# Optimization experiments

Hardware: AMD Instinct MI355X
Metric: run time of the kernel (lower is better)

Reference implementation:

```python
import jax, jax.numpy as jnp
import numpy as np

TOP_K = 2

def setup_inputs() -> dict:
    key = jax.random.key(0)
    k1, k2, k3, k4 = jax.random.split(key, 4)
    T, H, I, E = 8192, 2048, 4096, 8
    s = 0.02
    return {
        "hidden_states": jax.random.normal(k1, (T, H), dtype=jnp.float32),
        "router_w": jax.random.normal(k2, (E, H), dtype=jnp.float32) * s,
        "ws": jax.random.normal(k3, (E, 2 * I, H), dtype=jnp.float32) * s,  # [gate; up]
        "w2s": jax.random.normal(k4, (E, H, I), dtype=jnp.float32) * s,
    }

def reference(hidden_states, router_w, ws, w2s):
    # Router gating: softmax over experts, top-k, NO renormalization
    logits = hidden_states @ router_w.T              # [T, E]
    probs = jax.nn.softmax(logits, axis=-1)
    topv, topi = jax.lax.top_k(probs, TOP_K)         # [T, K]
    T, E = probs.shape
    I = w2s.shape[2]
    # Dense routing-weight matrix [T, E]; top_k indices are unique per token
    w = jnp.zeros_like(probs).at[jnp.arange(T)[:, None], topi].set(topv)
    out = jnp.zeros_like(hidden_states)
    for e in range(E):  # fixed small expert loop; avoids [T,E,2I] blowup
        gate = hidden_states @ ws[e, :I].T           # [T, I]
        up = hidden_states @ ws[e, I:].T             # [T, I]
        h = jax.nn.silu(gate) * up                   # SwiGLU
        out = out + w[:, e:e + 1] * (h @ w2s[e].T)   # combine
    return out
```

## Files before the change

### kernel.cpp

```cpp
#include <hip/hip_runtime.h>
#include <cstdint>
#include <cstddef>

#define T_TOK 8192
#define HDIM  2048
#define IDIM  4096
#define NEXP  8
#define MAXT  72

typedef __bf16 bf16x8 __attribute__((ext_vector_type(8)));
typedef float  f32x4  __attribute__((ext_vector_type(4)));

#define BARRIER() __builtin_amdgcn_s_barrier()
#define LGKM0()   do { asm volatile("s_waitcnt lgkmcnt(0)" ::: "memory"); __builtin_amdgcn_sched_barrier(0); } while (0)
#define VMW(n)    do { asm volatile("s_waitcnt vmcnt(" #n ")" ::: "memory"); } while (0)

__device__ __forceinline__ unsigned short f2bf(float f) {
    union { float f; unsigned u; } v; v.f = f;
    unsigned r = v.u + 0x7FFFu + ((v.u >> 16) & 1u);
    return (unsigned short)(r >> 16);
}

__device__ __forceinline__ void gload16(const void* g, void* l) {
    __builtin_amdgcn_global_load_lds((__attribute__((address_space(1))) void*)g,
                                     (__attribute__((address_space(3))) void*)l,
                                     16, 0, 0);
}

__global__ __launch_bounds__(256) void router_k(const float* __restrict__ hs,
                                                const float* __restrict__ rw,
                                                float* __restrict__ wgt,
                                                int* __restrict__ counts,
                                                int* __restrict__ lists) {
    int gid  = blockIdx.x * 256 + threadIdx.x;
    int tok  = gid >> 6;
    int lane = threadIdx.x & 63;
    const float* x = hs + (size_t)tok * HDIM;

    float acc[NEXP];
#pragma unroll
    for (int e = 0; e < NEXP; ++e) acc[e] = 0.f;
    for (int h = lane; h < HDIM; h += 64) {
        float xv = x[h];
#pragma unroll
        for (int e = 0; e < NEXP; ++e) acc[e] = fmaf(xv, rw[e * HDIM + h], acc[e]);
    }
#pragma unroll
    for (int off = 32; off > 0; off >>= 1) {
#pragma unroll
        for (int e = 0; e < NEXP; ++e) acc[e] += __shfl_xor(acc[e], off, 64);
    }
    if (lane == 0) {
        float m = acc[0];
#pragma unroll
        for (int e = 1; e < NEXP; ++e) m = fmaxf(m, acc[e]);
        float p[NEXP]; float s = 0.f;
#pragma unroll
        for (int e = 0; e < NEXP; ++e) { p[e] = expf(acc[e] - m); s += p[e]; }
        float inv = 1.f / s;
        int i1 = 0;
#pragma unroll
        for (int e = 1; e < NEXP; ++e) if (acc[e] > acc[i1]) i1 = e;
        int i2 = -1;
#pragma unroll
        for (int e = 0; e < NEXP; ++e) if (e != i1 && (i2 < 0 || acc[e] > acc[i2])) i2 = e;
#pragma unroll
        for (int e = 0; e < NEXP; ++e)
            wgt[(size_t)tok * NEXP + e] = (e == i1 || e == i2) ? p[e] * inv : 0.f;
        int p1 = atomicAdd(&counts[i1], 1);
        lists[i1 * T_TOK + p1] = tok;
        int p2 = atomicAdd(&counts[i2], 1);
        lists[i2 * T_TOK + p2] = (1 << 16) | tok;
    }
}

__global__ void plan_k(const int* __restrict__ counts, int* __restrict__ offs,
                       int* __restrict__ desc, int* __restrict__ ntiles) {
    if (threadIdx.x == 0 && blockIdx.x == 0) {
        int off = 0, n = 0;
        for (int e = 0; e < NEXP; ++e) {
            offs[e] = off;
            int nt = (counts[e] + 255) >> 8;
            for (int t = 0; t < nt; ++t) desc[n++] = (e << 16) | t;
            off += nt * 256;
        }
        *ntiles = n;
    }
}

__global__ __launch_bounds__(256) void cvt_k(const float* __restrict__ in,
                                             unsigned short* __restrict__ out, long n4) {
    long i      = (long)blockIdx.x * 256 + threadIdx.x;
    long stride = (long)gridDim.x * 256;
    const float4* in4 = (const float4*)in;
    ushort4* out4 = (ushort4*)out;
    for (long j = i; j < n4; j += stride) {
        float4 v = in4[j];
        ushort4 o;
        o.x = f2bf(v.x); o.y = f2bf(v.y); o.z = f2bf(v.z); o.w = f2bf(v.w);
        out4[j] = o;
    }
}

__global__ __launch_bounds__(512, 2) void gemm1_k(const unsigned short* __restrict__ A,
                                                  const unsigned short* __restrict__ Wall,
                                                  unsigned short* __restrict__ Hout,
                                                  const int* __restrict__ lists,
                                                  const int* __restrict__ counts,
                                                  const int* __restrict__ offs,
                                                  const int* __restrict__ desc,
                                                  const int* __restrict__ ntiles) {
    const int slot = blockIdx.y;
    if (slot >= *ntiles) return;
    const int dsc = desc[slot];
    const int e = dsc >> 16, tt = dsc & 0xFFFF;
    const int cnt = counts[e];
    const int t0 = tt * 256;
    const int* list = lists + e * T_TOK;
    const unsigned short* W = Wall + (size_t)e * 2 * IDIM * HDIM;
    const int hbase = offs[e];
    const int n0 = blockIdx.x * 128;

    extern __shared__ __align__(16) char lds[];

    const int tid  = threadIdx.x;
    const int lane = tid & 63;
    const int wid  = tid >> 6;
    const int wr   = wid >> 2;
    const int wc   = wid & 3;

    const int prow = tid >> 3;
    const int pcol = (tid & 7) * 16;
    const int fsw  = ((prow & 4) << 3) | ((prow & 8) << 3);
    const int lcol = (pcol ^ fsw) >> 1;
    unsigned aoff[4];
#pragma unroll
    for (int i = 0; i < 4; ++i) {
        int g = t0 + i * 64 + prow;
        int tok = list[(g < cnt) ? g : t0] & 0xFFFF;
        aoff[i] = (unsigned)tok * HDIM + lcol;
    }
    unsigned goff[2], uoff[2];
#pragma unroll
    for (int i = 0; i < 2; ++i) {
        goff[i] = (unsigned)(n0 + i * 64 + prow) * HDIM + lcol;
        uoff[i] = (unsigned)(IDIM + n0 + i * 64 + prow) * HDIM + lcol;
    }
    const int dst = tid * 16;

#define G1_STAGE(buf, kt) do {                                                     \
    unsigned k0_ = (unsigned)(kt) * 64;                                            \
    _Pragma("unroll") for (int i_ = 0; i_ < 4; ++i_)                               \
        gload16(A + aoff[i_] + k0_, lds + (buf) * 32768 + i_ * 8192 + dst);        \
    _Pragma("unroll") for (int i_ = 0; i_ < 2; ++i_)                               \
        gload16(W + goff[i_] + k0_, lds + 65536 + (buf) * 16384 + i_ * 8192 + dst);\
    _Pragma("unroll") for (int i_ = 0; i_ < 2; ++i_)                               \
        gload16(W + uoff[i_] + k0_, lds + 98304 + (buf) * 16384 + i_ * 8192 + dst);\
} while (0)

    const int frd = (lane & 12) << 3;
    const int cb0 = (((lane >> 4) * 16)      ) ^ frd;
    const int cb1 = (((lane >> 4) * 16) + 64 ) ^ frd;
    const int arow = wr * 16384 + (lane & 15) * 128;
    const int bgrow = 65536 + (wc * 32 + (lane & 15)) * 128;
    const int burow = 98304 + (wc * 32 + (lane & 15)) * 128;

    f32x4 accg[8][2], accu[8][2];
#pragma unroll
    for (int mi = 0; mi < 8; ++mi)
#pragma unroll
        for (int ni = 0; ni < 2; ++ni) {
            accg[mi][ni] = (f32x4){0.f, 0.f, 0.f, 0.f};
            accu[mi][ni] = (f32x4){0.f, 0.f, 0.f, 0.f};
        }

    G1_STAGE(0, 0);
    G1_STAGE(1, 1);
    VMW(8);
    BARRIER();

    const int NT = HDIM / 64;
    int buf = 0;
    for (int kt = 0; kt < NT; ++kt) {
        const char* la = lds + buf * 32768 + arow;
        const char* lg = lds + buf * 16384 + bgrow;
        const char* lu = lds + buf * 16384 + burow;
        bf16x8 af[2][4], bg[2][2], bu[2][2];
#pragma unroll
        for (int mi = 0; mi < 4; ++mi) {
            af[0][mi] = *(const bf16x8*)(la + mi * 2048 + cb0);
            af[1][mi] = *(const bf16x8*)(la + mi * 2048 + cb1);
        }
#pragma unroll
        for (int ni = 0; ni < 2; ++ni) {
            bg[0][ni] = *(const bf16x8*)(lg + ni * 2048 + cb0);
            bg[1][ni] = *(const bf16x8*)(lg + ni * 2048 + cb1);
            bu[0][ni] = *(const bf16x8*)(lu + ni * 2048 + cb0);
            bu[1][ni] = *(const bf16x8*)(lu + ni * 2048 + cb1);
        }
        LGKM0();
        __builtin_amdgcn_s_setprio(1);
#pragma unroll
        for (int ks = 0; ks < 2; ++ks)
#pragma unroll
            for (int mi = 0; mi < 4; ++mi)
#pragma unroll
                for (int ni = 0; ni < 2; ++ni)
                    accg[mi][ni] = __builtin_amdgcn_mfma_f32_16x16x32_bf16(af[ks][mi], bg[ks][ni], accg[mi][ni], 0, 0, 0);
        __builtin_amdgcn_s_setprio(0);
        BARRIER();
        __builtin_amdgcn_s_setprio(1);
#pragma unroll
        for (int ks = 0; ks < 2; ++ks)
#pragma unroll
            for (int mi = 0; mi < 4; ++mi)
#pragma unroll
                for (int ni = 0; ni < 2; ++ni)
                    accu[mi][ni] = __builtin_amdgcn_mfma_f32_16x16x32_bf16(af[ks][mi], bu[ks][ni], accu[mi][ni], 0, 0, 0);
        __builtin_amdgcn_s_setprio(0);
#pragma unroll
        for (int mi = 0; mi < 4; ++mi) {
            af[0][mi] = *(const bf16x8*)(la + (mi + 4) * 2048 + cb0);
            af[1][mi] = *(const bf16x8*)(la + (mi + 4) * 2048 + cb1);
        }
        LGKM0();
        __builtin_amdgcn_s_setprio(1);
#pragma unroll
        for (int ks = 0; ks < 2; ++ks)
#pragma unroll
            for (int mi = 0; mi < 4; ++mi)
#pragma unroll
                for (int ni = 0; ni < 2; ++ni)
                    accg[mi + 4][ni] = __builtin_amdgcn_mfma_f32_16x16x32_bf16(af[ks][mi], bg[ks][ni], accg[mi + 4][ni], 0, 0, 0);
        __builtin_amdgcn_s_setprio(0);
        BARRIER();
        G1_STAGE(buf, (kt + 2) & (NT - 1));
        __builtin_amdgcn_s_setprio(1);
#pragma unroll
        for (int ks = 0; ks < 2; ++ks)
#pragma unroll
            for (int mi = 0; mi < 4; ++mi)
#pragma unroll
                for (int ni = 0; ni < 2; ++ni)
                    accu[mi + 4][ni] = __builtin_amdgcn_mfma_f32_16x16x32_bf16(af[ks][mi], bu[ks][ni], accu[mi + 4][ni], 0, 0, 0);
        __builtin_amdgcn_s_setprio(0);
        VMW(8);
        BARRIER();
        buf ^= 1;
    }
    VMW(0);
#undef G1_STAGE

#pragma unroll
    for (int mi = 0; mi < 8; ++mi)
#pragma unroll
        for (int ni = 0; ni < 2; ++ni)
#pragma unroll
            for (int j = 0; j < 4; ++j) {
                int row = hbase + t0 + wr * 128 + mi * 16 + ((lane >> 4) << 2) + j;
                int col = n0 + wc * 32 + ni * 16 + (lane & 15);
                float g = accg[mi][ni][j], u = accu[mi][ni][j];
                float hv = (g / (1.f + expf(-g))) * u;
                Hout[(size_t)row * IDIM + col] = f2bf(hv);
            }
}

__global__ __launch_bounds__(512, 2) void gemm2_k(const unsigned short* __restrict__ Ah,
                                                  const unsigned short* __restrict__ Ball,
                                                  const float* __restrict__ wgt,
                                                  float* __restrict__ outP,
                                                  const int* __restrict__ lists,
                                                  const int* __restrict__ counts,
                                                  const int* __restrict__ offs,
                                                  const int* __restrict__ desc,
                                                  const int* __restrict__ ntiles) {
    const int slot = blockIdx.y;
    if (slot >= *ntiles) return;
    const int dsc = desc[slot];
    const int e = dsc >> 16, tt = dsc & 0xFFFF;
    const int cnt = counts[e];
    const int t0 = tt * 256;
    const int* list = lists + e * T_TOK;
    const unsigned short* B = Ball + (size_t)e * HDIM * IDIM;
    const int hbase = offs[e];
    const int n0 = blockIdx.x * 128;

    extern __shared__ __align__(16) char lds[];

    const int tid  = threadIdx.x;
    const int lane = tid & 63;
    const int wid  = tid >> 6;
    const int wr   = wid >> 2;
    const int wc   = wid & 3;

    const int prow = tid >> 3;
    const int pcol = (tid & 7) * 16;
    const int fsw  = ((prow & 4) << 3) | ((prow & 8) << 3);
    const int lcol = (pcol ^ fsw) >> 1;
    unsigned aoff[4];
#pragma unroll
    for (int i = 0; i < 4; ++i)
        aoff[i] = (unsigned)(hbase + t0 + i * 64 + prow) * IDIM + lcol;
    unsigned boff[2];
#pragma unroll
    for (int i = 0; i < 2; ++i)
        boff[i] = (unsigned)(n0 + i * 64 + prow) * IDIM + lcol;
    const int dst = tid * 16;

#define G2_STAGE(buf, kt) do {                                                     \
    unsigned k0_ = (unsigned)(kt) * 64;                                            \
    _Pragma("unroll") for (int i_ = 0; i_ < 4; ++i_)                               \
        gload16(Ah + aoff[i_] + k0_, lds + (buf) * 32768 + i_ * 8192 + dst);       \
    _Pragma("unroll") for (int i_ = 0; i_ < 2; ++i_)                               \
        gload16(B + boff[i_] + k0_, lds + 65536 + (buf) * 16384 + i_ * 8192 + dst);\
} while (0)

    const int frd = (lane & 12) << 3;
    const int cb0 = (((lane >> 4) * 16)      ) ^ frd;
    const int cb1 = (((lane >> 4) * 16) + 64 ) ^ frd;
    const int arow = wr * 16384 + (lane & 15) * 128;
    const int brow = 65536 + (wc * 32 + (lane & 15)) * 128;

    f32x4 acc[8][2];
#pragma unroll
    for (int mi = 0; mi < 8; ++mi)
#pragma unroll
        for (int ni = 0; ni < 2; ++ni) acc[mi][ni] = (f32x4){0.f, 0.f, 0.f, 0.f};

    G2_STAGE(0, 0);
    G2_STAGE(1, 1);
    VMW(6);
    BARRIER();

    const int NT = IDIM / 64;
    int buf = 0;
    for (int kt = 0; kt < NT; ++kt) {
        const char* la = lds + buf * 32768 + arow;
        const char* lb = lds + buf * 16384 + brow;
        bf16x8 af[2][4], bfr[2][2];
#pragma unroll
        for (int mi = 0; mi < 4; ++mi) {
            af[0][mi] = *(const bf16x8*)(la + mi * 2048 + cb0);
            af[1][mi] = *(const bf16x8*)(la + mi * 2048 + cb1);
        }
#pragma unroll
        for (int ni = 0; ni < 2; ++ni) {
            bfr[0][ni] = *(const bf16x8*)(lb + ni * 2048 + cb0);
            bfr[1][ni] = *(const bf16x8*)(lb + ni * 2048 + cb1);
        }
        LGKM0();
        __builtin_amdgcn_s_setprio(1);
#pragma unroll
        for (int ks = 0; ks < 2; ++ks)
#pragma unroll
            for (int mi = 0; mi < 4; ++mi)
#pragma unroll
                for (int ni = 0; ni < 2; ++ni)
                    acc[mi][ni] = __builtin_amdgcn_mfma_f32_16x16x32_bf16(af[ks][mi], bfr[ks][ni], acc[mi][ni], 0, 0, 0);
        __builtin_amdgcn_s_setprio(0);
        BARRIER();
#pragma unroll
        for (int mi = 0; mi < 4; ++mi) {
            af[0][mi] = *(const bf16x8*)(la + (mi + 4) * 2048 + cb0);
            af[1][mi] = *(const bf16x8*)(la + (mi + 4) * 2048 + cb1);
        }
        LGKM0();
        __builtin_amdgcn_s_setprio(1);
#pragma unroll
        for (int ks = 0; ks < 2; ++ks)
#pragma unroll
            for (int mi = 0; mi < 2; ++mi)
#pragma unroll
                for (int ni = 0; ni < 2; ++ni)
                    acc[mi + 4][ni] = __builtin_amdgcn_mfma_f32_16x16x32_bf16(af[ks][mi], bfr[ks][ni], acc[mi + 4][ni], 0, 0, 0);
        __builtin_amdgcn_s_setprio(0);
        BARRIER();
        G2_STAGE(buf, (kt + 2) & (NT - 1));
        __builtin_amdgcn_s_setprio(1);
#pragma unroll
        for (int ks = 0; ks < 2; ++ks)
#pragma unroll
            for (int mi = 2; mi < 4; ++mi)
#pragma unroll
                for (int ni = 0; ni < 2; ++ni)
                    acc[mi + 4][ni] = __builtin_amdgcn_mfma_f32_16x16x32_bf16(af[ks][mi], bfr[ks][ni], acc[mi + 4][ni], 0, 0, 0);
        __builtin_amdgcn_s_setprio(0);
        VMW(6);
        BARRIER();
        buf ^= 1;
    }
    VMW(0);
#undef G2_STAGE

#pragma unroll
    for (int mi = 0; mi < 8; ++mi)
#pragma unroll
        for (int j = 0; j < 4; ++j) {
            int g = t0 + wr * 128 + mi * 16 + ((lane >> 4) << 2) + j;
            if (g < cnt) {
                int ent = list[g];
                int tok = ent & 0xFFFF;
                int sl  = ent >> 16;
                float w = wgt[(size_t)tok * NEXP + e];
                float* o = outP + (size_t)sl * T_TOK * HDIM + (size_t)tok * HDIM;
#pragma unroll
                for (int ni = 0; ni < 2; ++ni) {
                    int col = n0 + wc * 32 + ni * 16 + (lane & 15);
                    o[col] = w * acc[mi][ni][j];
                }
            }
        }
}

__global__ __launch_bounds__(256) void combine_k(const float* __restrict__ p0,
                                                 const float* __restrict__ p1,
                                                 float* __restrict__ out, long n4) {
    long i      = (long)blockIdx.x * 256 + threadIdx.x;
    long stride = (long)gridDim.x * 256;
    const float4* a4 = (const float4*)p0;
    const float4* b4 = (const float4*)p1;
    float4* o4 = (float4*)out;
    for (long j = i; j < n4; j += stride) {
        float4 a = a4[j], b = b4[j];
        o4[j] = make_float4(a.x + b.x, a.y + b.y, a.z + b.z, a.w + b.w);
    }
}

extern "C" void kernel_launch(void* const* d_in, const int* in_sizes, int n_in,
                              void* d_out, int out_size, void* d_ws, size_t ws_size,
                              hipStream_t stream) {
    const float* hs  = (const float*)d_in[0];
    const float* rw  = (const float*)d_in[1];
    const float* ws  = (const float*)d_in[2];
    const float* w2s = (const float*)d_in[3];
    float* out = (float*)d_out;

    char* wsp = (char*)d_ws;
    unsigned short* hs_bf = (unsigned short*)(wsp);
    unsigned short* w_bf  = (unsigned short*)(wsp + 33554432ULL);
    unsigned short* w2_bf = (unsigned short*)(wsp + 301989888ULL);
    unsigned short* h_bf  = (unsigned short*)(wsp + 436207616ULL);
    float*          outP  = (float*)(wsp + 587202560ULL);
    float*          wgt   = (float*)(wsp + 721420288ULL);
    int*            counts = (int*)(wsp + 721682432ULL);
    int*            offs   = (int*)(wsp + 721682560ULL);
    int*            lists  = (int*)(wsp + 721682688ULL);
    int*            desc   = (int*)(wsp + 721944832ULL);
    int*            ntiles = (int*)(wsp + 721945344ULL);

    hipMemsetAsync(counts, 0, NEXP * sizeof(int), stream);
    cvt_k<<<2048, 256, 0, stream>>>(hs, hs_bf, (long)T_TOK * HDIM / 4);
    cvt_k<<<4096, 256, 0, stream>>>(ws, w_bf, (long)NEXP * 2 * IDIM * HDIM / 4);
    cvt_k<<<4096, 256, 0, stream>>>(w2s, w2_bf, (long)NEXP * HDIM * IDIM / 4);
    router_k<<<(T_TOK * 64) / 256, 256, 0, stream>>>(hs, rw, wgt, counts, lists);
    plan_k<<<1, 64, 0, stream>>>(counts, offs, desc, ntiles);

    gemm1_k<<<dim3(IDIM / 128, MAXT), 512, 131072, stream>>>(
        hs_bf, w_bf, h_bf, lists, counts, offs, desc, ntiles);
    gemm2_k<<<dim3(HDIM / 128, MAXT), 512, 98304, stream>>>(
        h_bf, w2_bf, wgt, outP, lists, counts, offs, desc, ntiles);
    combine_k<<<2048, 256, 0, stream>>>(outP, outP + (size_t)T_TOK * HDIM, out,
                                        (long)T_TOK * HDIM / 4);
}
```

Baseline: 1.592 ms.

## Widen gemm2 N-tile to 256, change LDS swizzle, restructure MFMA k-slicing

gemm2 now computes a 256-column tile per block instead of 128, doubling accumulators and B staging so each loaded A tile is reused across more output columns and fewer blocks are launched. Both GEMMs switch to a full 3-bit XOR swizzle on LDS rows to reduce bank conflicts. The inner loop is rewritten to load one k-half of fragments at a time and interleave gate and up MFMAs, which also removes one barrier per iteration. This lowers register pressure for fragments, but the larger gemm2 tile raises accumulator registers and LDS use, which may lower occupancy, and gemm2 now has fewer blocks to spread across the CUs.

```diff
diff --git a/kernel.cpp b/kernel.cpp
--- a/kernel.cpp
+++ b/kernel.cpp
@@ -14,6 +14,8 @@
 #define BARRIER() __builtin_amdgcn_s_barrier()
 #define LGKM0()   do { asm volatile("s_waitcnt lgkmcnt(0)" ::: "memory"); __builtin_amdgcn_sched_barrier(0); } while (0)
 #define VMW(n)    do { asm volatile("s_waitcnt vmcnt(" #n ")" ::: "memory"); } while (0)
+#define PRIO1()   __builtin_amdgcn_s_setprio(1)
+#define PRIO0()   __builtin_amdgcn_s_setprio(0)
 
 __device__ __forceinline__ unsigned short f2bf(float f) {
     union { float f; unsigned u; } v; v.f = f;
@@ -131,8 +133,7 @@
 
     const int prow = tid >> 3;
     const int pcol = (tid & 7) * 16;
-    const int fsw  = ((prow & 4) << 3) | ((prow & 8) << 3);
-    const int lcol = (pcol ^ fsw) >> 1;
+    const int lcol = (pcol ^ ((prow & 7) << 4)) >> 1;
     unsigned aoff[4];
 #pragma unroll
     for (int i = 0; i < 4; ++i) {
@@ -158,12 +159,11 @@
         gload16(W + uoff[i_] + k0_, lds + 98304 + (buf) * 16384 + i_ * 8192 + dst);\
 } while (0)
 
-    const int frd = (lane & 12) << 3;
-    const int cb0 = (((lane >> 4) * 16)      ) ^ frd;
-    const int cb1 = (((lane >> 4) * 16) + 64 ) ^ frd;
+    const int frd = (lane & 7) << 4;
+    const int cb0 = (((lane >> 4) * 16)     ) ^ frd;
+    const int cb1 = (((lane >> 4) * 16) | 64) ^ frd;
     const int arow = wr * 16384 + (lane & 15) * 128;
-    const int bgrow = 65536 + (wc * 32 + (lane & 15)) * 128;
-    const int burow = 98304 + (wc * 32 + (lane & 15)) * 128;
+    const int brow = (wc * 32 + (lane & 15)) * 128;
 
     f32x4 accg[8][2], accu[8][2];
 #pragma unroll
@@ -183,67 +183,66 @@
     int buf = 0;
     for (int kt = 0; kt < NT; ++kt) {
         const char* la = lds + buf * 32768 + arow;
-        const char* lg = lds + buf * 16384 + bgrow;
-        const char* lu = lds + buf * 16384 + burow;
-        bf16x8 af[2][4], bg[2][2], bu[2][2];
-#pragma unroll
-        for (int mi = 0; mi < 4; ++mi) {
-            af[0][mi] = *(const bf16x8*)(la + mi * 2048 + cb0);
-            af[1][mi] = *(const bf16x8*)(la + mi * 2048 + cb1);
+        const char* lg = lds + 65536 + buf * 16384 + brow;
+        const char* lu = lds + 98304 + buf * 16384 + brow;
+        bf16x8 af[4], bg[2], bu[2];
+#pragma unroll
+        for (int mi = 0; mi < 4; ++mi) af[mi] = *(const bf16x8*)(la + mi * 2048 + cb0);
+#pragma unroll
+        for (int ni = 0; ni < 2; ++ni) {
+            bg[ni] = *(const bf16x8*)(lg + ni * 2048 + cb0);
+            bu[ni] = *(const bf16x8*)(lu + ni * 2048 + cb0);
         }
+        LGKM0(); PRIO1();
+#pragma unroll
+        for (int mi = 0; mi < 4; ++mi)
+#pragma unroll
+            for (int ni = 0; ni < 2; ++ni) {
+                accg[mi][ni] = __builtin_amdgcn_mfma_f32_16x16x32_bf16(af[mi], bg[ni], accg[mi][ni], 0, 0, 0);
+                accu[mi][ni] = __builtin_amdgcn_mfma_f32_16x16x32_bf16(af[mi], bu[ni], accu[mi][ni], 0, 0, 0);
+            }
+        PRIO0();
+#pragma unroll
+        for (int mi = 0; mi < 4; ++mi) af[mi] = *(const bf16x8*)(la + (mi + 4) * 2048 + cb0);
+        LGKM0(); PRIO1();
+#pragma unroll
+        for (int mi = 0; mi < 4; ++mi)
+#pragma unroll
+            for (int ni = 0; ni < 2; ++ni) {
+                accg[mi + 4][ni] = __builtin_amdgcn_mfma_f32_16x16x32_bf16(af[mi], bg[ni], accg[mi + 4][ni], 0, 0, 0);
+                accu[mi + 4][ni] = __builtin_amdgcn_mfma_f32_16x16x32_bf16(af[mi], bu[ni], accu[mi + 4][ni], 0, 0, 0);
+            }
+        PRIO0();
+#pragma unroll
+        for (int mi = 0; mi < 4; ++mi) af[mi] = *(const bf16x8*)(la + mi * 2048 + cb1);
 #pragma unroll
         for (int ni = 0; ni < 2; ++ni) {
-            bg[0][ni] = *(const bf16x8*)(lg + ni * 2048 + cb0);
-            bg[1][ni] = *(const bf16x8*)(lg + ni * 2048 + cb1);
-            bu[0][ni] = *(const bf16x8*)(lu + ni * 2048 + cb0);
-            bu[1][ni] = *(const bf16x8*)(lu + ni * 2048 + cb1);
+            bg[ni] = *(const bf16x8*)(lg + ni * 2048 + cb1);
+            bu[ni] = *(const bf16x8*)(lu + ni * 2048 + cb1);
         }
+        LGKM0(); PRIO1();
+#pragma unroll
+        for (int mi = 0; mi < 4; ++mi)
+#pragma unroll
+            for (int ni = 0; ni < 2; ++ni) {
+                accg[mi][ni] = __builtin_amdgcn_mfma_f32_16x16x32_bf16(af[mi], bg[ni], accg[mi][ni], 0, 0, 0);
+                accu[mi][ni] = __builtin_amdgcn_mfma_f32_16x16x32_bf16(af[mi], bu[ni], accu[mi][ni], 0, 0, 0);
+            }
+        PRIO0();
+#pragma unroll
+        for (int mi = 0; mi < 4; ++mi) af[mi] = *(const bf16x8*)(la + (mi + 4) * 2048 + cb1);
         LGKM0();
-        __builtin_amdgcn_s_setprio(1);
-#pragma unroll
-        for (int ks = 0; ks < 2; ++ks)
-#pragma unroll
-            for (int mi = 0; mi < 4; ++mi)
-#pragma unroll
-                for (int ni = 0; ni < 2; ++ni)
-                    accg[mi][ni] = __builtin_amdgcn_mfma_f32_16x16x32_bf16(af[ks][mi], bg[ks][ni], accg[mi][ni], 0, 0, 0);
-        __builtin_amdgcn_s_setprio(0);
-        BARRIER();
-        __builtin_amdgcn_s_setprio(1);
-#pragma unroll
-        for (int ks = 0; ks < 2; ++ks)
-#pragma unroll
-            for (int mi = 0; mi < 4; ++mi)
-#pragma unroll
-                for (int ni = 0; ni < 2; ++ni)
-                    accu[mi][ni] = __builtin_amdgcn_mfma_f32_16x16x32_bf16(af[ks][mi], bu[ks][ni], accu[mi][ni], 0, 0, 0);
-        __builtin_amdgcn_s_setprio(0);
-#pragma unroll
-        for (int mi = 0; mi < 4; ++mi) {
-            af[0][mi] = *(const bf16x8*)(la + (mi + 4) * 2048 + cb0);
-            af[1][mi] = *(const bf16x8*)(la + (mi + 4) * 2048 + cb1);
-        }
-        LGKM0();
-        __builtin_amdgcn_s_setprio(1);
-#pragma unroll
-        for (int ks = 0; ks < 2; ++ks)
-#pragma unroll
-            for (int mi = 0; mi < 4; ++mi)
-#pragma unroll
-                for (int ni = 0; ni < 2; ++ni)
-                    accg[mi + 4][ni] = __builtin_amdgcn_mfma_f32_16x16x32_bf16(af[ks][mi], bg[ks][ni], accg[mi + 4][ni], 0, 0, 0);
-        __builtin_amdgcn_s_setprio(0);
         BARRIER();
         G1_STAGE(buf, (kt + 2) & (NT - 1));
-        __builtin_amdgcn_s_setprio(1);
-#pragma unroll
-        for (int ks = 0; ks < 2; ++ks)
-#pragma unroll
-            for (int mi = 0; mi < 4; ++mi)
-#pragma unroll
-                for (int ni = 0; ni < 2; ++ni)
-                    accu[mi + 4][ni] = __builtin_amdgcn_mfma_f32_16x16x32_bf16(af[ks][mi], bu[ks][ni], accu[mi + 4][ni], 0, 0, 0);
-        __builtin_amdgcn_s_setprio(0);
+        PRIO1();
+#pragma unroll
+        for (int mi = 0; mi < 4; ++mi)
+#pragma unroll
+            for (int ni = 0; ni < 2; ++ni) {
+                accg[mi + 4][ni] = __builtin_amdgcn_mfma_f32_16x16x32_bf16(af[mi], bg[ni], accg[mi + 4][ni], 0, 0, 0);
+                accu[mi + 4][ni] = __builtin_amdgcn_mfma_f32_16x16x32_bf16(af[mi], bu[ni], accu[mi + 4][ni], 0, 0, 0);
+            }
+        PRIO0();
         VMW(8);
         BARRIER();
         buf ^= 1;
@@ -283,7 +282,7 @@
     const int* list = lists + e * T_TOK;
     const unsigned short* B = Ball + (size_t)e * HDIM * IDIM;
     const int hbase = offs[e];
-    const int n0 = blockIdx.x * 128;
+    const int n0 = blockIdx.x * 256;
 
     extern __shared__ __align__(16) char lds[];
 
@@ -295,97 +294,90 @@
 
     const int prow = tid >> 3;
     const int pcol = (tid & 7) * 16;
-    const int fsw  = ((prow & 4) << 3) | ((prow & 8) << 3);
-    const int lcol = (pcol ^ fsw) >> 1;
-    unsigned aoff[4];
-#pragma unroll
-    for (int i = 0; i < 4; ++i)
+    const int lcol = (pcol ^ ((prow & 7) << 4)) >> 1;
+    unsigned aoff[4], boff[4];
+#pragma unroll
+    for (int i = 0; i < 4; ++i) {
         aoff[i] = (unsigned)(hbase + t0 + i * 64 + prow) * IDIM + lcol;
-    unsigned boff[2];
-#pragma unroll
-    for (int i = 0; i < 2; ++i)
         boff[i] = (unsigned)(n0 + i * 64 + prow) * IDIM + lcol;
+    }
     const int dst = tid * 16;
 
 #define G2_STAGE(buf, kt) do {                                                     \
     unsigned k0_ = (unsigned)(kt) * 64;                                            \
     _Pragma("unroll") for (int i_ = 0; i_ < 4; ++i_)                               \
         gload16(Ah + aoff[i_] + k0_, lds + (buf) * 32768 + i_ * 8192 + dst);       \
-    _Pragma("unroll") for (int i_ = 0; i_ < 2; ++i_)                               \
-        gload16(B + boff[i_] + k0_, lds + 65536 + (buf) * 16384 + i_ * 8192 + dst);\
+    _Pragma("unroll") for (int i_ = 0; i_ < 4; ++i_)                               \
+        gload16(B + boff[i_] + k0_, lds + 65536 + (buf) * 32768 + i_ * 8192 + dst);\
 } while (0)
 
-    const int frd = (lane & 12) << 3;
-    const int cb0 = (((lane >> 4) * 16)      ) ^ frd;
-    const int cb1 = (((lane >> 4) * 16) + 64 ) ^ frd;
+    const int frd = (lane & 7) << 4;
+    const int cb0 = (((lane >> 4) * 16)     ) ^ frd;
+    const int cb1 = (((lane >> 4) * 16) | 64) ^ frd;
     const int arow = wr * 16384 + (lane & 15) * 128;
-    const int brow = 65536 + (wc * 32 + (lane & 15)) * 128;
-
-    f32x4 acc[8][2];
+    const int brow = (wc * 64 + (lane & 15)) * 128;
+
+    f32x4 acc[8][4];
 #pragma unroll
     for (int mi = 0; mi < 8; ++mi)
 #pragma unroll
-        for (int ni = 0; ni < 2; ++ni) acc[mi][ni] = (f32x4){0.f, 0.f, 0.f, 0.f};
+        for (int ni = 0; ni < 4; ++ni) acc[mi][ni] = (f32x4){0.f, 0.f, 0.f, 0.f};
 
     G2_STAGE(0, 0);
     G2_STAGE(1, 1);
-    VMW(6);
+    VMW(8);
     BARRIER();
 
     const int NT = IDIM / 64;
     int buf = 0;
     for (int kt = 0; kt < NT; ++kt) {
         const char* la = lds + buf * 32768 + arow;
-        const char* lb = lds + buf * 16384 + brow;
-        bf16x8 af[2][4], bfr[2][2];
-#pragma unroll
-        for (int mi = 0; mi < 4; ++mi) {
-            af[0][mi] = *(const bf16x8*)(la + mi * 2048 + cb0);
-            af[1][mi] = *(const bf16x8*)(la + mi * 2048 + cb1);
-        }
-#pragma unroll
-        for (int ni = 0; ni < 2; ++ni) {
-            bfr[0][ni] = *(const bf16x8*)(lb + ni * 2048 + cb0);
-            bfr[1][ni] = *(const bf16x8*)(lb + ni * 2048 + cb1);
-        }
+        const char* lb = lds + 65536 + buf * 32768 + brow;
+        bf16x8 af[4], bfr[4];
+#pragma unroll
+        for (int mi = 0; mi < 4; ++mi) af[mi] = *(const bf16x8*)(la + mi * 2048 + cb0);
+#pragma unroll
+        for (int ni = 0; ni < 4; ++ni) bfr[ni] = *(const bf16x8*)(lb + ni * 2048 + cb0);
+        LGKM0(); PRIO1();
+#pragma unroll
+        for (int mi = 0; mi < 4; ++mi)
+#pragma unroll
+            for (int ni = 0; ni < 4; ++ni)
+                acc[mi][ni] = __builtin_amdgcn_mfma_f32_16x16x32_bf16(af[mi], bfr[ni], acc[mi][ni], 0, 0, 0);
+        PRIO0();
+#pragma unroll
+        for (int mi = 0; mi < 4; ++mi) af[mi] = *(const bf16x8*)(la + (mi + 4) * 2048 + cb0);
+        LGKM0(); PRIO1();
+#pragma unroll
+        for (int mi = 0; mi < 4; ++mi)
+#pragma unroll
+            for (int ni = 0; ni < 4; ++ni)
+                acc[mi + 4][ni] = __builtin_amdgcn_mfma_f32_16x16x32_bf16(af[mi], bfr[ni], acc[mi + 4][ni], 0, 0, 0);
+        PRIO0();
+#pragma unroll
+        for (int mi = 0; mi < 4; ++mi) af[mi] = *(const bf16x8*)(la + mi * 2048 + cb1);
+#pragma unroll
+        for (int ni = 0; ni < 4; ++ni) bfr[ni] = *(const bf16x8*)(lb + ni * 2048 + cb1);
+        LGKM0(); PRIO1();
+#pragma unroll
+        for (int mi = 0; mi < 4; ++mi)
+#pragma unroll
+            for (int ni = 0; ni < 4; ++ni)
+                acc[mi][ni] = __builtin_amdgcn_mfma_f32_16x16x32_bf16(af[mi], bfr[ni], acc[mi][ni], 0, 0, 0);
+        PRIO0();
+#pragma unroll
+        for (int mi = 0; mi < 4; ++mi) af[mi] = *(const bf16x8*)(la + (mi + 4) * 2048 + cb1);
         LGKM0();
-        __builtin_amdgcn_s_setprio(1);
-#pragma unroll
-        for (int ks = 0; ks < 2; ++ks)
-#pragma unroll
-            for (int mi = 0; mi < 4; ++mi)
-#pragma unroll
-                for (int ni = 0; ni < 2; ++ni)
-                    acc[mi][ni] = __builtin_amdgcn_mfma_f32_16x16x32_bf16(af[ks][mi], bfr[ks][ni], acc[mi][ni], 0, 0, 0);
-        __builtin_amdgcn_s_setprio(0);
-        BARRIER();
-#pragma unroll
-        for (int mi = 0; mi < 4; ++mi) {
-            af[0][mi] = *(const bf16x8*)(la + (mi + 4) * 2048 + cb0);
-            af[1][mi] = *(const bf16x8*)(la + (mi + 4) * 2048 + cb1);
-        }
-        LGKM0();
-        __builtin_amdgcn_s_setprio(1);
-#pragma unroll
-        for (int ks = 0; ks < 2; ++ks)
-#pragma unroll
-            for (int mi = 0; mi < 2; ++mi)
-#pragma unroll
-                for (int ni = 0; ni < 2; ++ni)
-                    acc[mi + 4][ni] = __builtin_amdgcn_mfma_f32_16x16x32_bf16(af[ks][mi], bfr[ks][ni], acc[mi + 4][ni], 0, 0, 0);
-        __builtin_amdgcn_s_setprio(0);
         BARRIER();
         G2_STAGE(buf, (kt + 2) & (NT - 1));
-        __builtin_amdgcn_s_setprio(1);
-#pragma unroll
-        for (int ks = 0; ks < 2; ++ks)
-#pragma unroll
-            for (int mi = 2; mi < 4; ++mi)
-#pragma unroll
-                for (int ni = 0; ni < 2; ++ni)
-                    acc[mi + 4][ni] = __builtin_amdgcn_mfma_f32_16x16x32_bf16(af[ks][mi], bfr[ks][ni], acc[mi + 4][ni], 0, 0, 0);
-        __builtin_amdgcn_s_setprio(0);
-        VMW(6);
+        PRIO1();
+#pragma unroll
+        for (int mi = 0; mi < 4; ++mi)
+#pragma unroll
+            for (int ni = 0; ni < 4; ++ni)
+                acc[mi + 4][ni] = __builtin_amdgcn_mfma_f32_16x16x32_bf16(af[mi], bfr[ni], acc[mi + 4][ni], 0, 0, 0);
+        PRIO0();
+        VMW(8);
         BARRIER();
         buf ^= 1;
     }
@@ -404,8 +396,8 @@
                 float w = wgt[(size_t)tok * NEXP + e];
                 float* o = outP + (size_t)sl * T_TOK * HDIM + (size_t)tok * HDIM;
 #pragma unroll
-                for (int ni = 0; ni < 2; ++ni) {
-                    int col = n0 + wc * 32 + ni * 16 + (lane & 15);
+                for (int ni = 0; ni < 4; ++ni) {
+                    int col = n0 + wc * 64 + ni * 16 + (lane & 15);
                     o[col] = w * acc[mi][ni][j];
                 }
             }
@@ -457,7 +449,7 @@
 
     gemm1_k<<<dim3(IDIM / 128, MAXT), 512, 131072, stream>>>(
         hs_bf, w_bf, h_bf, lists, counts, offs, desc, ntiles);
-    gemm2_k<<<dim3(HDIM / 128, MAXT), 512, 98304, stream>>>(
+    gemm2_k<<<dim3(HDIM / 256, MAXT), 512, 131072, stream>>>(
         h_bf, w2_bf, wgt, outP, lists, counts, offs, desc, ntiles);
     combine_k<<<2048, 256, 0, stream>>>(outP, outP + (size_t)T_TOK * HDIM, out,
                                         (long)T_TOK * HDIM / 4);
```

After: 1.494 ms. 6.2% less time.
